# Performance work log

Hardware: AMD Instinct MI355X
Metric: run time of the kernel (lower is better)

## Reference

```python
import jax, jax.numpy as jnp
import numpy as np

B, T, S = 64, 128, 128
E, H, D, K = 512, 1024, 1024, 1024  # embed, hidden, decoder_size, encoder.output_size
IN2 = 2 * D + 2 * H  # output_rnn input size


def gru_cell(x, h, Wih, Whh, bih, bhh):
    # PyTorch GRUCell math; gate order (r, z, n)
    gi = x @ Wih.T + bih
    gh = h @ Whh.T + bhh
    i_r, i_z, i_n = jnp.split(gi, 3, axis=-1)
    h_r, h_z, h_n = jnp.split(gh, 3, axis=-1)
    r = jax.nn.sigmoid(i_r + h_r)
    z = jax.nn.sigmoid(i_z + h_z)
    n = jnp.tanh(i_n + r * h_n)
    return (1.0 - z) * n + z * h


def setup_inputs() -> dict:
    key = jax.random.key(0)
    ks = jax.random.split(key, 24)
    p = 0.05
    rn = lambda k, s, sc=1.0: jax.random.normal(k, s, jnp.float32) * sc
    return {
        'reversed_input': rn(ks[0], (B, T, E)),
        'y_length': jnp.full((B,), T, jnp.int32),
        'mask': jnp.ones((B, T), bool),
        'y_states': rn(ks[1], (B, T, D)),
        'encoder_output': rn(ks[2], (B, S, K)),
        'src_mask': jnp.ones((B, 1, S), bool),
        # backward-reading GRU (self.rnn)
        'rnn_Wih': rn(ks[3], (3 * H, E), p), 'rnn_Whh': rn(ks[4], (3 * H, H), p),
        'rnn_bih': rn(ks[5], (3 * H,), p), 'rnn_bhh': rn(ks[6], (3 * H,), p),
        # output_rnn GRU
        'out_Wih': rn(ks[7], (3 * H, IN2), p), 'out_Whh': rn(ks[8], (3 * H, H), p),
        'out_bih': rn(ks[9], (3 * H,), p), 'out_bhh': rn(ks[10], (3 * H,), p),
        'corr_W': rn(ks[11], (D, H), p), 'corr_b': rn(ks[12], (D,), p),
        'reward_W': rn(ks[13], (2, H), p), 'reward_b': rn(ks[14], (2,), p),
        'attv_W': rn(ks[15], (H, H + K), p), 'attv_b': rn(ks[16], (H,), p),
        # Bahdanau attention (bias-free linears)
        'key_W': rn(ks[17], (H, K), p), 'query_W': rn(ks[18], (H, H), p),
        'energy_W': rn(ks[19], (1, H), p),
    }


def reference(reversed_input, y_length, mask, y_states, encoder_output, src_mask,
              rnn_Wih, rnn_Whh, rnn_bih, rnn_bhh,
              out_Wih, out_Whh, out_bih, out_bhh,
              corr_W, corr_b, reward_W, reward_b,
              attv_W, attv_b, key_W, query_W, energy_W):
    b, t, _ = reversed_input.shape
    h_dim = rnn_Whh.shape[1]
    d_dim = corr_W.shape[0]
    dt = reversed_input.dtype

    # _apply_rnn: step-by-step GRU over reversed input == full GRU scan
    def rnn_step(h, x):
        h = gru_cell(x, h, rnn_Wih, rnn_Whh, rnn_bih, rnn_bhh)
        return h, h
    h0 = jnp.zeros((b, h_dim), dt)
    _, rnn_outs = jax.lax.scan(rnn_step, h0, reversed_input.transpose(1, 0, 2))
    rnn_outputs = jnp.flip(rnn_outs.transpose(1, 0, 2), axis=1)  # [B,T,H]

    proj_keys = encoder_output @ key_W.T  # [B,S,H] precomputed attention keys
    comb_states = jnp.concatenate([y_states, rnn_outputs], axis=-1)  # [B,T,D+H]
    sm = src_mask[:, 0, :]  # [B,S]

    def step(carry, comb_t):
        h, corr_prev, att_prev = carry
        inp = jnp.concatenate([comb_t, corr_prev, att_prev], axis=-1)  # [B,2D+2H]
        h = gru_cell(inp, h, out_Wih, out_Whh, out_bih, out_bhh)  # rnn_output == hidden[-1]
        corr = jnp.tanh(h @ corr_W.T + corr_b)  # corr_activation=tanh
        reward = h @ reward_W.T + reward_b  # [B,2]
        reward_pred = jax.lax.stop_gradient(jnp.argmax(reward, axis=-1)).astype(dt)[:, None]
        # Bahdanau attention: v^T tanh(Wq q + Wk k)
        pq = h @ query_W.T  # [B,H]
        energies = jnp.tanh(pq[:, None, :] + proj_keys) @ energy_W[0]  # [B,S]
        scores = jnp.where(sm, energies, -jnp.inf)
        alphas = jax.nn.softmax(scores, axis=-1)
        context = jnp.einsum('bs,bsk->bk', alphas, encoder_output)
        att_vec = jnp.tanh(jnp.concatenate([h, context], axis=-1) @ attv_W.T + attv_b)
        corr = corr * (1.0 - reward_pred)
        return (h, corr, att_vec), (corr, reward, alphas)

    init = (jnp.zeros((b, h_dim), dt), jnp.zeros((b, d_dim), dt), jnp.zeros((b, h_dim), dt))
    _, (corrs, rewards, attns) = jax.lax.scan(step, init, comb_states.transpose(1, 0, 2))
    return (corrs.transpose(1, 0, 2), rewards.transpose(1, 0, 2), attns.transpose(1, 0, 2))
```

## Files before the change

### kernel.cpp

```cpp
#include <hip/hip_runtime.h>
#include <hip/hip_bf16.h>
#include <math.h>

#define B 64
#define T 128
#define S 128
#define E 512
#define H 1024
#define D 1024
#define KDIM 1024
#define G3 3072
#define JT 16

__device__ __forceinline__ float sigmoidf_(float x) { return 1.f / (1.f + expf(-x)); }

template<int SRC>
__global__ __launch_bounds__(256) void gemm128(
    const float* __restrict__ A1, const float* __restrict__ A2, int lda,
    const float* __restrict__ W, int ldw, const float* __restrict__ bias,
    float* __restrict__ C, int ldc, int Kd, int c0, int chLog) {
  __shared__ __align__(16) float As[16][132];
  __shared__ __align__(16) float Ws[16][132];
  const int bm = blockIdx.y * 128;
  const int bn = blockIdx.x * 128;
  const int tid = threadIdx.x;
  const int tr = tid >> 4, tc = tid & 15;
  float acc[8][8];
#pragma unroll
  for (int i = 0; i < 8; ++i)
#pragma unroll
    for (int j = 0; j < 8; ++j) acc[i][j] = 0.f;

  for (int k0 = 0; k0 < Kd; k0 += 16) {
#pragma unroll
    for (int l = 0; l < 8; ++l) {
      int i = tid + l * 256;
      int r = i >> 4, kk = i & 15;
      int rg = bm + r;
      int k = k0 + kk;
      float v;
      if (SRC == 0) {
        v = A1[(size_t)rg * lda + k];
      } else {
        int b = rg >> chLog, tl = rg & ((1 << chLog) - 1);
        int trow = b * T + c0 + tl;
        if (SRC == 1) v = A1[(size_t)trow * E + k];
        else v = (k < 1024) ? A1[(size_t)trow * 1024 + k]
                            : A2[(size_t)trow * 1024 + (k - 1024)];
      }
      As[kk][r] = v;
    }
#pragma unroll
    for (int l = 0; l < 8; ++l) {
      int i = tid + l * 256;
      int c = i >> 4, kk = i & 15;
      Ws[kk][c] = W[(size_t)(bn + c) * ldw + k0 + kk];
    }
    __syncthreads();
#pragma unroll
    for (int kk = 0; kk < 16; ++kk) {
      float a[8], w[8];
      *(float4*)&a[0] = *(const float4*)&As[kk][tr * 8];
      *(float4*)&a[4] = *(const float4*)&As[kk][tr * 8 + 4];
      *(float4*)&w[0] = *(const float4*)&Ws[kk][tc * 8];
      *(float4*)&w[4] = *(const float4*)&Ws[kk][tc * 8 + 4];
#pragma unroll
      for (int i = 0; i < 8; ++i)
#pragma unroll
        for (int j = 0; j < 8; ++j)
          acc[i][j] = fmaf(a[i], w[j], acc[i][j]);
    }
    __syncthreads();
  }
#pragma unroll
  for (int i = 0; i < 8; ++i) {
    int rg = bm + tr * 8 + i;
#pragma unroll
    for (int j = 0; j < 8; ++j) {
      int cc = bn + tc * 8 + j;
      float bv = bias ? bias[cc] : 0.f;
      C[(size_t)rg * ldc + cc] = acc[i][j] + bv;
    }
  }
}

struct SBSeg { const float* A; const float* W; int lda; int ldw; int N; };
struct SBArgs { SBSeg s[6]; };

__global__ __launch_bounds__(256) void sb_gemm(SBArgs args, int jtPerSeg, int Nstr,
                                               float* __restrict__ part) {
  const int seg = blockIdx.x / jtPerSeg;
  const int jt = blockIdx.x % jtPerSeg;
  const SBSeg sg = args.s[seg];
  const int j0 = jt * JT;
  if (j0 >= sg.N) return;
  const int wv = __builtin_amdgcn_readfirstlane(threadIdx.x >> 6);
  const int lane = threadIdx.x & 63;
  float acc[JT];
#pragma unroll
  for (int jj = 0; jj < JT; ++jj) acc[jj] = 0.f;
#pragma unroll 1
  for (int half = 0; half < 2; ++half) {
    const int kw = wv * 128 + half * 64;
    float a[64];
    const float4* ap = (const float4*)(sg.A + (size_t)lane * sg.lda + kw);
#pragma unroll
    for (int q = 0; q < 16; ++q) {
      float4 v = ap[q];
      a[q * 4 + 0] = v.x; a[q * 4 + 1] = v.y; a[q * 4 + 2] = v.z; a[q * 4 + 3] = v.w;
    }
#pragma unroll
    for (int jj = 0; jj < JT; ++jj) {
      int j = j0 + jj;
      if (j < sg.N) {
        const float4* wp = (const float4*)(sg.W + (size_t)j * sg.ldw + kw);
        float s0 = 0.f, s1 = 0.f, s2 = 0.f, s3 = 0.f;
#pragma unroll
        for (int q = 0; q < 16; ++q) {
          float4 w4 = wp[q];
          s0 = fmaf(a[q * 4 + 0], w4.x, s0);
          s1 = fmaf(a[q * 4 + 1], w4.y, s1);
          s2 = fmaf(a[q * 4 + 2], w4.z, s2);
          s3 = fmaf(a[q * 4 + 3], w4.w, s3);
        }
        acc[jj] += (s0 + s1) + (s2 + s3);
      }
    }
  }
  __shared__ float red[4][JT][64];
#pragma unroll
  for (int jj = 0; jj < JT; ++jj) red[wv][jj][lane] = acc[jj];
  __syncthreads();
  for (int idx = threadIdx.x; idx < JT * 64; idx += 256) {
    int b = idx >> 4, jj = idx & 15;
    int j = j0 + jj;
    if (j < sg.N) {
      float v = red[0][jj][b] + red[1][jj][b] + red[2][jj][b] + red[3][jj][b];
      part[((size_t)seg * 64 + b) * Nstr + j] = v;
    }
  }
}

__global__ __launch_bounds__(256) void gru_reduce(
    const float* __restrict__ part, const float* __restrict__ gi,
    int CH, int tl, int nsGi, int ghStart, int nsGh,
    const float* __restrict__ bhh, float* __restrict__ hrow,
    float* __restrict__ flip_out, int t) {
  const int b = blockIdx.x >> 2;
  const int j = (blockIdx.x & 3) * 256 + threadIdx.x;
  const float* gb = gi + (size_t)(b * CH + tl) * G3;
  float gir = gb[j];
  float giz = gb[H + j];
  float gin = gb[2 * H + j];
  for (int p2 = 0; p2 < nsGi; ++p2) {
    const float* pp = part + ((size_t)p2 * 64 + b) * G3;
    gir += pp[j]; giz += pp[H + j]; gin += pp[2 * H + j];
  }
  float ghr = bhh[j], ghz = bhh[H + j], ghn = bhh[2 * H + j];
  for (int p2 = ghStart; p2 < ghStart + nsGh; ++p2) {
    const float* pp = part + ((size_t)p2 * 64 + b) * G3;
    ghr += pp[j]; ghz += pp[H + j]; ghn += pp[2 * H + j];
  }
  float r = sigmoidf_(gir + ghr);
  float z = sigmoidf_(giz + ghz);
  float n = tanhf(gin + r * ghn);
  float hold = hrow[(size_t)b * H + j];
  float hnew = (1.f - z) * n + z * hold;
  hrow[(size_t)b * H + j] = hnew;
  if (flip_out)
    flip_out[(size_t)b * T * H + (size_t)(T - 1 - t) * H + j] = hnew;
}

__global__ __launch_bounds__(256) void hproj_gemm(
    const float* __restrict__ h,
    const float* __restrict__ corrW, const float* __restrict__ corrB,
    const float* __restrict__ qW, const float* __restrict__ avW,
    const float* __restrict__ rewW, const float* __restrict__ rewB,
    float* __restrict__ corrR, float* __restrict__ pq,
    float* __restrict__ attH, float* __restrict__ rew,
    float* __restrict__ out_rewards, int t) {
  const int task = blockIdx.x;
  const int tid = threadIdx.x;
  const int wv = __builtin_amdgcn_readfirstlane(tid >> 6);
  const int lane = tid & 63;
  const float* Wb; int ldw = 1024, n0, nrows, typ;
  if (task < 128)      { Wb = corrW; n0 = task * 8;         nrows = 8; typ = 0; }
  else if (task < 256) { Wb = qW;    n0 = (task - 128) * 8; nrows = 8; typ = 1; }
  else if (task < 384) { Wb = avW;   n0 = (task - 256) * 8; nrows = 8; typ = 2; ldw = 2048; }
  else                 { Wb = rewW;  n0 = 0;                nrows = 2; typ = 3; }
  const int k0 = wv * 256;
  const float* arow = h + (size_t)lane * H + k0;
  float acc[8] = {0.f, 0.f, 0.f, 0.f, 0.f, 0.f, 0.f, 0.f};
  for (int sc = 0; sc < 8; ++sc) {
    float av[32];
    const float4* ap = (const float4*)(arow + sc * 32);
#pragma unroll
    for (int q = 0; q < 8; ++q) {
      float4 v = ap[q];
      av[4*q] = v.x; av[4*q+1] = v.y; av[4*q+2] = v.z; av[4*q+3] = v.w;
    }
#pragma unroll
    for (int rr = 0; rr < 8; ++rr) {
      if (rr < nrows) {
        const float4* wp = (const float4*)(Wb + (size_t)(n0 + rr) * ldw + k0 + sc * 32);
        float s = acc[rr];
#pragma unroll
        for (int q = 0; q < 8; ++q) {
          float4 w = wp[q];
          s = fmaf(av[4*q],   w.x, s);
          s = fmaf(av[4*q+1], w.y, s);
          s = fmaf(av[4*q+2], w.z, s);
          s = fmaf(av[4*q+3], w.w, s);
        }
        acc[rr] = s;
      }
    }
  }
  __shared__ float red[4][8][64];
#pragma unroll
  for (int rr = 0; rr < 8; ++rr) red[wv][rr][lane] = acc[rr];
  __syncthreads();
  for (int idx = tid; idx < 512; idx += 256) {
    int b = idx >> 3, jj = idx & 7;
    if (jj < nrows) {
      int n = n0 + jj;
      float v = red[0][jj][b] + red[1][jj][b] + red[2][jj][b] + red[3][jj][b];
      if (typ == 0) corrR[(size_t)b * 1024 + n] = v + corrB[n];
      else if (typ == 1) pq[(size_t)b * 1024 + n] = v;
      else if (typ == 2) attH[(size_t)n * 64 + b] = v;
      else {
        float rv = v + rewB[n];
        rew[n * 64 + b] = rv;
        out_rewards[((size_t)b * T + t) * 2 + n] = rv;
      }
    }
  }
}

__global__ __launch_bounds__(256) void energy_kernel(
    const float* __restrict__ pq, const float* __restrict__ pk,
    const float* __restrict__ eW, float* __restrict__ energies) {
  int wid = blockIdx.x * 4 + (threadIdx.x >> 6);
  int lane = threadIdx.x & 63;
  int b = wid >> 7, s = wid & 127;
  const float* pkp = pk + ((size_t)b * S + s) * H;
  const float* qp = pq + (size_t)b * H;
  float acc = 0.f;
#pragma unroll
  for (int i = 0; i < 16; ++i) {
    int j = lane + i * 64;
    acc += tanhf(qp[j] + pkp[j]) * eW[j];
  }
#pragma unroll
  for (int off = 32; off > 0; off >>= 1) acc += __shfl_down(acc, off);
  if (lane == 0) energies[b * S + s] = acc;
}

__global__ __launch_bounds__(256) void smct_plus(
    const float* __restrict__ energies, const float* __restrict__ enc,
    const float* __restrict__ corrR, const float* __restrict__ rew,
    float* __restrict__ ctx, float* __restrict__ uv,
    float* __restrict__ out_attns, float* __restrict__ out_corrs, int t) {
  int b = blockIdx.x, kt = blockIdx.y;
  int tid = threadIdx.x;
  __shared__ float se[128], sa[128], ss[128];
  if (tid < 128) { se[tid] = energies[b * S + tid]; sa[tid] = se[tid]; }
  __syncthreads();
  for (int st2 = 64; st2 > 0; st2 >>= 1) {
    if (tid < st2) sa[tid] = fmaxf(sa[tid], sa[tid + st2]);
    __syncthreads();
  }
  float mx = sa[0];
  __syncthreads();
  if (tid < 128) { sa[tid] = expf(se[tid] - mx); ss[tid] = sa[tid]; }
  __syncthreads();
  for (int st2 = 64; st2 > 0; st2 >>= 1) {
    if (tid < st2) ss[tid] += ss[tid + st2];
    __syncthreads();
  }
  float inv = 1.f / ss[0];
  __syncthreads();
  if (tid < 128) sa[tid] *= inv;
  __syncthreads();
  int k = kt * 256 + tid;
  const float* eb = enc + (size_t)b * S * KDIM + k;
  float acc = 0.f;
#pragma unroll 4
  for (int s2 = 0; s2 < S; ++s2) acc = fmaf(sa[s2], eb[(size_t)s2 * KDIM], acc);
  ctx[(size_t)b * KDIM + k] = acc;
  float r0 = rew[b], r1 = rew[64 + b];
  float g = (r1 > r0) ? 0.f : 1.f;
  float cv = g * tanhf(corrR[(size_t)b * 1024 + k]);
  uv[(size_t)b * 2048 + k] = cv;
  out_corrs[((size_t)b * T + t) * D + k] = cv;
  if (kt == 0 && tid < 128) out_attns[((size_t)b * T + t) * S + tid] = sa[tid];
}

__global__ __launch_bounds__(256) void final_attv(
    const float* __restrict__ attH, const float* __restrict__ avW,
    const float* __restrict__ avB, const float* __restrict__ ctx,
    float* __restrict__ uv) {
  const int n0 = blockIdx.x * 8;
  const int tid = threadIdx.x;
  const int wv = __builtin_amdgcn_readfirstlane(tid >> 6);
  const int lane = tid & 63;
  __shared__ float red[4][8][64];
  float acc[8];
#pragma unroll
  for (int jj = 0; jj < 8; ++jj) acc[jj] = 0.f;
  const int k0 = wv * 256;
  const float* arow = ctx + (size_t)lane * KDIM + k0;
  for (int sc = 0; sc < 8; ++sc) {
    float av[32];
    const float4* ap = (const float4*)(arow + sc * 32);
#pragma unroll
    for (int q = 0; q < 8; ++q) {
      float4 v = ap[q];
      av[4*q] = v.x; av[4*q+1] = v.y; av[4*q+2] = v.z; av[4*q+3] = v.w;
    }
#pragma unroll
    for (int jj = 0; jj < 8; ++jj) {
      const float4* wp = (const float4*)(avW + (size_t)(n0 + jj) * 2048 + 1024 + k0 + sc * 32);
      float s = acc[jj];
#pragma unroll
      for (int q = 0; q < 8; ++q) {
        float4 w = wp[q];
        s = fmaf(av[4*q],   w.x, s);
        s = fmaf(av[4*q+1], w.y, s);
        s = fmaf(av[4*q+2], w.z, s);
        s = fmaf(av[4*q+3], w.w, s);
      }
      acc[jj] = s;
    }
  }
#pragma unroll
  for (int jj = 0; jj < 8; ++jj) red[wv][jj][lane] = acc[jj];
  __syncthreads();
  for (int idx = tid; idx < 512; idx += 256) {
    int jj = idx >> 6, bb = idx & 63;
    int n = n0 + jj;
    float v = red[0][jj][bb] + red[1][jj][bb] + red[2][jj][bb] + red[3][jj][bb]
            + attH[(size_t)n * 64 + bb] + avB[n];
    uv[(size_t)bb * 2048 + 1024 + n] = tanhf(v);
  }
}

extern "C" void kernel_launch(void* const* d_in, const int* in_sizes, int n_in,
                              void* d_out, int out_size, void* d_ws, size_t ws_size,
                              hipStream_t stream) {
  const float* reversed_input = (const float*)d_in[0];
  const float* y_states = (const float*)d_in[3];
  const float* encoder = (const float*)d_in[4];
  const float* rnn_Wih = (const float*)d_in[6];
  const float* rnn_Whh = (const float*)d_in[7];
  const float* rnn_bih = (const float*)d_in[8];
  const float* rnn_bhh = (const float*)d_in[9];
  const float* out_Wih = (const float*)d_in[10];
  const float* out_Whh = (const float*)d_in[11];
  const float* out_bih = (const float*)d_in[12];
  const float* out_bhh = (const float*)d_in[13];
  const float* corr_W = (const float*)d_in[14];
  const float* corr_b = (const float*)d_in[15];
  const float* reward_W = (const float*)d_in[16];
  const float* reward_b = (const float*)d_in[17];
  const float* attv_W = (const float*)d_in[18];
  const float* attv_b = (const float*)d_in[19];
  const float* key_W = (const float*)d_in[20];
  const float* query_W = (const float*)d_in[21];
  const float* energy_W = (const float*)d_in[22];

  float* out_corrs = (float*)d_out;
  float* out_rewards = out_corrs + (size_t)B * T * D;
  float* out_attns = out_rewards + (size_t)B * T * 2;

  float* p = (float*)d_ws;
  float* rnn_flip = p;  p += (size_t)B * T * H;
  float* proj_keys = p; p += (size_t)B * S * H;
  float* part = p;      p += (size_t)6 * 64 * G3;
  float* h = p;         p += (size_t)B * H;
  float* uv = p;        p += (size_t)B * 2048;
  float* ctx = p;       p += (size_t)B * KDIM;
  float* corrR = p;     p += (size_t)B * 1024;
  float* pq = p;        p += (size_t)B * H;
  float* attH = p;      p += (size_t)H * 64;
  float* rew = p;       p += 128;
  float* energ = p;     p += (size_t)B * S;
  size_t fixedF = (size_t)(p - (float*)d_ws);
  int CH = 8, chLog = 3;
  {
    int c = 32, l = 5;
    for (; c >= 8; c >>= 1, --l)
      if (ws_size >= (fixedF + (size_t)c * 64 * G3) * 4) break;
    if (c < 8) { c = 8; l = 3; }
    CH = c; chLog = l;
  }
  float* gibuf = p;

  hipMemsetAsync(h, 0, (size_t)B * H * sizeof(float), stream);
  hipMemsetAsync(uv, 0, (size_t)B * 2048 * sizeof(float), stream);

  dim3 blk(256);

  gemm128<0><<<dim3(H / 128, (B * S) / 128), blk, 0, stream>>>(
      encoder, nullptr, KDIM, key_W, KDIM, nullptr, proj_keys, H, KDIM, 0, 0);

  for (int c0 = 0; c0 < T; c0 += CH) {
    gemm128<1><<<dim3(G3 / 128, (64 * CH) / 128), blk, 0, stream>>>(
        reversed_input, nullptr, 0, rnn_Wih, E, rnn_bih, gibuf, G3, E, c0, chLog);
    for (int tl = 0; tl < CH; ++tl) {
      int t = c0 + tl;
      SBArgs s1{};
      s1.s[0] = { h, rnn_Whh, H, H, G3 };
      s1.s[1] = { h + 512, rnn_Whh + 512, H, H, G3 };
      sb_gemm<<<2 * 192, blk, 0, stream>>>(s1, 192, G3, part);
      gru_reduce<<<256, blk, 0, stream>>>(part, gibuf, CH, tl, 0, 0, 2,
                                          rnn_bhh, h, rnn_flip, t);
    }
  }

  hipMemsetAsync(h, 0, (size_t)B * H * sizeof(float), stream);
  for (int c0 = 0; c0 < T; c0 += CH) {
    gemm128<2><<<dim3(G3 / 128, (64 * CH) / 128), blk, 0, stream>>>(
        y_states, rnn_flip, 0, out_Wih, 4096, out_bih, gibuf, G3, 2048, c0, chLog);
    for (int tl = 0; tl < CH; ++tl) {
      int t = c0 + tl;
      SBArgs k1{};
      for (int s2 = 0; s2 < 4; ++s2)
        k1.s[s2] = { uv + s2 * 512, out_Wih + 2048 + s2 * 512, 2048, 4096, G3 };
      for (int s2 = 0; s2 < 2; ++s2)
        k1.s[4 + s2] = { h + s2 * 512, out_Whh + s2 * 512, H, H, G3 };
      sb_gemm<<<6 * 192, blk, 0, stream>>>(k1, 192, G3, part);
      gru_reduce<<<256, blk, 0, stream>>>(part, gibuf, CH, tl, 4, 4, 2,
                                          out_bhh, h, nullptr, t);
      hproj_gemm<<<385, blk, 0, stream>>>(h, corr_W, corr_b, query_W, attv_W,
                                          reward_W, reward_b, corrR, pq, attH,
                                          rew, out_rewards, t);
      energy_kernel<<<2048, blk, 0, stream>>>(pq, proj_keys, energy_W, energ);
      smct_plus<<<dim3(B, 4), blk, 0, stream>>>(energ, encoder, corrR, rew,
                                                ctx, uv, out_attns, out_corrs, t);
      final_attv<<<128, blk, 0, stream>>>(attH, attv_W, attv_b, ctx, uv);
    }
  }
}
```

Before: 22.92 ms.

## Fold next-chunk input-gate GEMM into per-step recurrent gate kernel with double buffering

The per-chunk input projection GEMM (x @ Wih) is split into small 128x32 tiles. A slice of those tiles rides along as extra blocks in each timestep's recurrent gate kernel, writing into a second gi buffer for the next chunk. This removes the separate serialized chunk GEMM launches and uses idle CUs during the latency-bound recurrent steps. The cost is double the gi workspace, and a fallback path is kept when the workspace is too small. The rider tiles use a smaller, less efficient tile shape and may lengthen each step kernel.

```diff
diff --git a/kernel.cpp b/kernel.cpp
--- a/kernel.cpp
+++ b/kernel.cpp
@@ -85,35 +85,45 @@
 }
 
 struct SBSeg { const float* A; const float* W; int lda; int ldw; int N; };
-struct SBArgs { SBSeg s[6]; };
-
-__global__ __launch_bounds__(256) void sb_gemm(SBArgs args, int jtPerSeg, int Nstr,
-                                               float* __restrict__ part) {
-  const int seg = blockIdx.x / jtPerSeg;
-  const int jt = blockIdx.x % jtPerSeg;
-  const SBSeg sg = args.s[seg];
-  const int j0 = jt * JT;
-  if (j0 >= sg.N) return;
-  const int wv = __builtin_amdgcn_readfirstlane(threadIdx.x >> 6);
-  const int lane = threadIdx.x & 63;
-  float acc[JT];
-#pragma unroll
-  for (int jj = 0; jj < JT; ++jj) acc[jj] = 0.f;
+struct GPArgs {
+  SBSeg s[6];
+  int nGates;
+  int jtPerSeg;
+  float* part;
+  int ksel;
+  const float* rA1; const float* rA2;
+  const float* rW; const float* rBias;
+  float* rDst;
+  int rKd; int rLdw; int rC0; int chLog;
+  int tileBase;
+};
+
+__global__ __launch_bounds__(256) void gates_plus(GPArgs g) {
+  __shared__ __align__(16) float smem[4 * JT * 64];
+  const int tid = threadIdx.x;
+  if ((int)blockIdx.x < g.nGates) {
+    const int seg = blockIdx.x / g.jtPerSeg;
+    const int jt = blockIdx.x % g.jtPerSeg;
+    const SBSeg sg = g.s[seg];
+    const int j0 = jt * JT;
+    const int wv = __builtin_amdgcn_readfirstlane(tid >> 6);
+    const int lane = tid & 63;
+    float acc[JT];
+#pragma unroll
+    for (int jj = 0; jj < JT; ++jj) acc[jj] = 0.f;
 #pragma unroll 1
-  for (int half = 0; half < 2; ++half) {
-    const int kw = wv * 128 + half * 64;
-    float a[64];
-    const float4* ap = (const float4*)(sg.A + (size_t)lane * sg.lda + kw);
-#pragma unroll
-    for (int q = 0; q < 16; ++q) {
-      float4 v = ap[q];
-      a[q * 4 + 0] = v.x; a[q * 4 + 1] = v.y; a[q * 4 + 2] = v.z; a[q * 4 + 3] = v.w;
-    }
-#pragma unroll
-    for (int jj = 0; jj < JT; ++jj) {
-      int j = j0 + jj;
-      if (j < sg.N) {
-        const float4* wp = (const float4*)(sg.W + (size_t)j * sg.ldw + kw);
+    for (int half = 0; half < 2; ++half) {
+      const int kw = wv * 128 + half * 64;
+      float a[64];
+      const float4* ap = (const float4*)(sg.A + (size_t)lane * sg.lda + kw);
+#pragma unroll
+      for (int q = 0; q < 16; ++q) {
+        float4 v = ap[q];
+        a[q * 4 + 0] = v.x; a[q * 4 + 1] = v.y; a[q * 4 + 2] = v.z; a[q * 4 + 3] = v.w;
+      }
+#pragma unroll
+      for (int jj = 0; jj < JT; ++jj) {
+        const float4* wp = (const float4*)(sg.W + (size_t)(j0 + jj) * sg.ldw + kw);
         float s0 = 0.f, s1 = 0.f, s2 = 0.f, s3 = 0.f;
 #pragma unroll
         for (int q = 0; q < 16; ++q) {
@@ -126,17 +136,76 @@
         acc[jj] += (s0 + s1) + (s2 + s3);
       }
     }
-  }
-  __shared__ float red[4][JT][64];
-#pragma unroll
-  for (int jj = 0; jj < JT; ++jj) red[wv][jj][lane] = acc[jj];
-  __syncthreads();
-  for (int idx = threadIdx.x; idx < JT * 64; idx += 256) {
-    int b = idx >> 4, jj = idx & 15;
-    int j = j0 + jj;
-    if (j < sg.N) {
-      float v = red[0][jj][b] + red[1][jj][b] + red[2][jj][b] + red[3][jj][b];
-      part[((size_t)seg * 64 + b) * Nstr + j] = v;
+    float* red = smem;
+#pragma unroll
+    for (int jj = 0; jj < JT; ++jj) red[(wv * JT + jj) * 64 + lane] = acc[jj];
+    __syncthreads();
+    for (int idx = tid; idx < JT * 64; idx += 256) {
+      int b = idx >> 4, jj = idx & 15;
+      float v = red[(0 * JT + jj) * 64 + b] + red[(1 * JT + jj) * 64 + b] +
+                red[(2 * JT + jj) * 64 + b] + red[(3 * JT + jj) * 64 + b];
+      g.part[((size_t)seg * 64 + b) * G3 + j0 + jj] = v;
+    }
+  } else {
+    const int tile = g.tileBase + ((int)blockIdx.x - g.nGates);
+    const int rowT = tile / 96;
+    const int colT = tile % 96;
+    const int n0 = colT * 32;
+    float* As = smem;
+    float* Ws = smem + 16 * 132;
+    const int tr = tid >> 3;
+    const int tc = tid & 7;
+    float acc[4][4];
+#pragma unroll
+    for (int i = 0; i < 4; ++i)
+#pragma unroll
+      for (int j = 0; j < 4; ++j) acc[i][j] = 0.f;
+    const int chMask = (1 << g.chLog) - 1;
+    for (int k0 = 0; k0 < g.rKd; k0 += 16) {
+#pragma unroll
+      for (int l = 0; l < 8; ++l) {
+        int i = tid + l * 256;
+        int rr = i >> 4, kk = i & 15;
+        int rg = rowT * 128 + rr;
+        int b = rg >> g.chLog, tl2 = rg & chMask;
+        int trow = b * T + g.rC0 + tl2;
+        int k = k0 + kk;
+        float v;
+        if (g.ksel == 1) v = g.rA1[(size_t)trow * E + k];
+        else v = (k < 1024) ? g.rA1[(size_t)trow * 1024 + k]
+                            : g.rA2[(size_t)trow * 1024 + (k - 1024)];
+        As[kk * 132 + rr] = v;
+      }
+      {
+        int i = tid;
+        int c = i >> 4, kk = i & 15;
+        Ws[kk * 36 + c] = g.rW[(size_t)(n0 + c) * g.rLdw + k0 + kk];
+        i = tid + 256;
+        c = i >> 4; kk = i & 15;
+        Ws[kk * 36 + c] = g.rW[(size_t)(n0 + c) * g.rLdw + k0 + kk];
+      }
+      __syncthreads();
+#pragma unroll
+      for (int kk = 0; kk < 16; ++kk) {
+        float a[4], w[4];
+        *(float4*)&a[0] = *(const float4*)&As[kk * 132 + tr * 4];
+        *(float4*)&w[0] = *(const float4*)&Ws[kk * 36 + tc * 4];
+#pragma unroll
+        for (int i = 0; i < 4; ++i)
+#pragma unroll
+          for (int j = 0; j < 4; ++j)
+            acc[i][j] = fmaf(a[i], w[j], acc[i][j]);
+      }
+      __syncthreads();
+    }
+#pragma unroll
+    for (int i = 0; i < 4; ++i) {
+      int rg = rowT * 128 + tr * 4 + i;
+#pragma unroll
+      for (int j = 0; j < 4; ++j) {
+        int n = n0 + tc * 4 + j;
+        g.rDst[(size_t)rg * G3 + n] = acc[i][j] + g.rBias[n];
+      }
     }
   }
 }
@@ -386,51 +455,79 @@
   float* rew = p;       p += 128;
   float* energ = p;     p += (size_t)B * S;
   size_t fixedF = (size_t)(p - (float*)d_ws);
-  int CH = 8, chLog = 3;
+  int CH = 8, chLog = 3, dbuf = 0;
   {
     int c = 32, l = 5;
     for (; c >= 8; c >>= 1, --l)
-      if (ws_size >= (fixedF + (size_t)c * 64 * G3) * 4) break;
-    if (c < 8) { c = 8; l = 3; }
+      if (ws_size >= (fixedF + 2ull * c * 64 * G3) * 4) { dbuf = 1; break; }
+    if (!dbuf) { c = 8; l = 3; }
     CH = c; chLog = l;
   }
-  float* gibuf = p;
+  float* gibuf0 = p;  p += (size_t)CH * 64 * G3;
+  float* gibuf1 = dbuf ? p : gibuf0;
 
   hipMemsetAsync(h, 0, (size_t)B * H * sizeof(float), stream);
   hipMemsetAsync(uv, 0, (size_t)B * 2048 * sizeof(float), stream);
 
   dim3 blk(256);
+  const int nChunks = T / CH;
 
   gemm128<0><<<dim3(H / 128, (B * S) / 128), blk, 0, stream>>>(
       encoder, nullptr, KDIM, key_W, KDIM, nullptr, proj_keys, H, KDIM, 0, 0);
 
-  for (int c0 = 0; c0 < T; c0 += CH) {
-    gemm128<1><<<dim3(G3 / 128, (64 * CH) / 128), blk, 0, stream>>>(
-        reversed_input, nullptr, 0, rnn_Wih, E, rnn_bih, gibuf, G3, E, c0, chLog);
+  gemm128<1><<<dim3(G3 / 128, (64 * CH) / 128), blk, 0, stream>>>(
+      reversed_input, nullptr, 0, rnn_Wih, E, rnn_bih, gibuf0, G3, E, 0, chLog);
+  for (int c = 0; c < nChunks; ++c) {
+    int c0 = c * CH;
+    float* cur = (c & 1) ? gibuf1 : gibuf0;
+    float* nxt = (c & 1) ? gibuf0 : gibuf1;
+    int rider = (dbuf && c + 1 < nChunks) ? 1 : 0;
     for (int tl = 0; tl < CH; ++tl) {
       int t = c0 + tl;
-      SBArgs s1{};
-      s1.s[0] = { h, rnn_Whh, H, H, G3 };
-      s1.s[1] = { h + 512, rnn_Whh + 512, H, H, G3 };
-      sb_gemm<<<2 * 192, blk, 0, stream>>>(s1, 192, G3, part);
-      gru_reduce<<<256, blk, 0, stream>>>(part, gibuf, CH, tl, 0, 0, 2,
+      GPArgs g{};
+      g.s[0] = { h, rnn_Whh, H, H, G3 };
+      g.s[1] = { h + 512, rnn_Whh + 512, H, H, G3 };
+      g.nGates = 2 * 192; g.jtPerSeg = 192; g.part = part;
+      if (rider) {
+        g.ksel = 1; g.rA1 = reversed_input; g.rA2 = nullptr;
+        g.rW = rnn_Wih; g.rBias = rnn_bih; g.rDst = nxt;
+        g.rKd = E; g.rLdw = E; g.rC0 = c0 + CH; g.chLog = chLog;
+        g.tileBase = tl * 48;
+      }
+      gates_plus<<<2 * 192 + (rider ? 48 : 0), blk, 0, stream>>>(g);
+      gru_reduce<<<256, blk, 0, stream>>>(part, cur, CH, tl, 0, 0, 2,
                                           rnn_bhh, h, rnn_flip, t);
     }
+    if (!dbuf && c + 1 < nChunks)
+      gemm128<1><<<dim3(G3 / 128, (64 * CH) / 128), blk, 0, stream>>>(
+          reversed_input, nullptr, 0, rnn_Wih, E, rnn_bih, gibuf0, G3, E,
+          c0 + CH, chLog);
   }
 
   hipMemsetAsync(h, 0, (size_t)B * H * sizeof(float), stream);
-  for (int c0 = 0; c0 < T; c0 += CH) {
-    gemm128<2><<<dim3(G3 / 128, (64 * CH) / 128), blk, 0, stream>>>(
-        y_states, rnn_flip, 0, out_Wih, 4096, out_bih, gibuf, G3, 2048, c0, chLog);
+  gemm128<2><<<dim3(G3 / 128, (64 * CH) / 128), blk, 0, stream>>>(
+      y_states, rnn_flip, 0, out_Wih, 4096, out_bih, gibuf0, G3, 2048, 0, chLog);
+  for (int c = 0; c < nChunks; ++c) {
+    int c0 = c * CH;
+    float* cur = (c & 1) ? gibuf1 : gibuf0;
+    float* nxt = (c & 1) ? gibuf0 : gibuf1;
+    int rider = (dbuf && c + 1 < nChunks) ? 1 : 0;
     for (int tl = 0; tl < CH; ++tl) {
       int t = c0 + tl;
-      SBArgs k1{};
+      GPArgs g{};
       for (int s2 = 0; s2 < 4; ++s2)
-        k1.s[s2] = { uv + s2 * 512, out_Wih + 2048 + s2 * 512, 2048, 4096, G3 };
+        g.s[s2] = { uv + s2 * 512, out_Wih + 2048 + s2 * 512, 2048, 4096, G3 };
       for (int s2 = 0; s2 < 2; ++s2)
-        k1.s[4 + s2] = { h + s2 * 512, out_Whh + s2 * 512, H, H, G3 };
-      sb_gemm<<<6 * 192, blk, 0, stream>>>(k1, 192, G3, part);
-      gru_reduce<<<256, blk, 0, stream>>>(part, gibuf, CH, tl, 4, 4, 2,
+        g.s[4 + s2] = { h + s2 * 512, out_Whh + s2 * 512, H, H, G3 };
+      g.nGates = 6 * 192; g.jtPerSeg = 192; g.part = part;
+      if (rider) {
+        g.ksel = 2; g.rA1 = y_states; g.rA2 = rnn_flip;
+        g.rW = out_Wih; g.rBias = out_bih; g.rDst = nxt;
+        g.rKd = 2048; g.rLdw = 4096; g.rC0 = c0 + CH; g.chLog = chLog;
+        g.tileBase = tl * 48;
+      }
+      gates_plus<<<6 * 192 + (rider ? 48 : 0), blk, 0, stream>>>(g);
+      gru_reduce<<<256, blk, 0, stream>>>(part, cur, CH, tl, 4, 4, 2,
                                           out_bhh, h, nullptr, t);
       hproj_gemm<<<385, blk, 0, stream>>>(h, corr_W, corr_b, query_W, attv_W,
                                           reward_W, reward_b, corrR, pq, attH,
@@ -440,5 +537,9 @@
                                                 ctx, uv, out_attns, out_corrs, t);
       final_attv<<<128, blk, 0, stream>>>(attH, attv_W, attv_b, ctx, uv);
     }
-  }
-}
+    if (!dbuf && c + 1 < nChunks)
+      gemm128<2><<<dim3(G3 / 128, (64 * CH) / 128), blk, 0, stream>>>(
+          y_states, rnn_flip, 0, out_Wih, 4096, out_bih, gibuf0, G3, 2048,
+          c0 + CH, chLog);
+  }
+}
```

Measured after the change: 70.71 ms. +208.4%, slower.
